# Kernel tuning notes

Measured on AMD Instinct MI355X. Metric: run time of the kernel, lower is better.

Reference implementation:

```python
import jax, jax.numpy as jnp
import numpy as np

ALPHA_POS, ALPHA_NEG, GAMMA, TAU = 1.0, 2.0, 2.0, 0.7
LAMBDA_CP, MU_ECE, N_BINS = 6.0, 5.0, 15
N = 16777216


def setup_inputs() -> dict:
    key = jax.random.key(0)
    k1, k2, k3 = jax.random.split(key, 3)
    p_hat = jax.random.uniform(k1, (N,), dtype=jnp.float32)
    u_hat = jax.random.uniform(k2, (N,), dtype=jnp.float32)
    targets = jax.random.randint(k3, (N,), 0, 2, dtype=jnp.int32)
    return {"p_hat": p_hat, "u_hat": u_hat, "targets": targets}


def _ece(probs, labels):
    # bin b covers (b/n_bins, (b+1)/n_bins]; single-pass histogram via segment_sum
    bins = jnp.clip(jnp.ceil(probs * N_BINS).astype(jnp.int32) - 1, 0, N_BINS - 1)
    sum_p = jax.ops.segment_sum(probs, bins, num_segments=N_BINS)
    sum_y = jax.ops.segment_sum(labels, bins, num_segments=N_BINS)
    # (|I_b|/N)*|mean_y - mean_p| == |sum_y - sum_p| / N ; empty bins contribute 0
    n = probs.shape[0]
    return jnp.sum(jnp.abs(sum_y - sum_p)) / n


def reference(p_hat, u_hat, targets):
    t = targets.astype(p_hat.dtype)
    pos = targets == 1
    pt = jnp.where(pos, p_hat, 1.0 - p_hat)
    alpha = jnp.where(pos, ALPHA_POS, ALPHA_NEG)
    focal = jnp.mean(-alpha * (1.0 - pt) ** GAMMA * jnp.log(pt + 1e-12))

    mask_ow = (~pos) & (p_hat > TAU)   # overconfident wrong
    mask_uc = pos & (p_hat < TAU)      # underconfident correct
    penalty = jnp.where(mask_ow, (1.0 - u_hat) ** 2,
                        jnp.where(mask_uc, u_hat ** 2, 0.0))
    cp_loss = jnp.mean(penalty)

    ece = _ece(p_hat, t)
    return focal + LAMBDA_CP * cp_loss + MU_ECE * ece
```

## Files before the change

### kernel.cpp

```cpp
#include <hip/hip_runtime.h>

#define NB 15
#define NV 17
#define GRID 1024
#define BLOCK 256


__device__ __forceinline__ void process_elem(float pk, float uk, int tk,
                                             float& facc, float& cacc,
                                             float* bins)
{
    bool pos = (tk == 1);

    float pt    = pos ? pk : 1.0f - pk;
    float alpha = pos ? 1.0f : 2.0f;
    float om    = 1.0f - pt;
    facc -= alpha * om * om * __logf(pt + 1e-12f);

    float w   = 1.0f - uk;
    float pen = pos ? ((pk < 0.7f) ? uk * uk : 0.0f)
                    : ((pk > 0.7f) ? w * w : 0.0f);
    cacc += pen;

    int b = (int)ceilf(pk * 15.0f) - 1;
    b = (b < 0) ? 0 : ((b > NB - 1) ? NB - 1 : b);
    float v = (pos ? 1.0f : 0.0f) - pk;
    #pragma unroll
    for (int j = 0; j < NB; ++j)
        bins[j] += (b == j) ? v : 0.0f;
}

__global__ __launch_bounds__(BLOCK) void fcl_main(
    const float* __restrict__ p_hat,
    const float* __restrict__ u_hat,
    const int*   __restrict__ targets,
    float* __restrict__ partials,
    int n4, int n)
{
    float bins[NB];
    #pragma unroll
    for (int j = 0; j < NB; ++j) bins[j] = 0.0f;
    float facc = 0.0f, cacc = 0.0f;

    const float4* __restrict__ p4 = (const float4*)p_hat;
    const float4* __restrict__ u4 = (const float4*)u_hat;
    const int4*   __restrict__ t4 = (const int4*)targets;

    const int stride = gridDim.x * blockDim.x;
    int i = blockIdx.x * blockDim.x + threadIdx.x;

    for (; i + stride < n4; i += 2 * stride) {
        float4 p0 = p4[i];          float4 p1 = p4[i + stride];
        float4 u0 = u4[i];          float4 u1 = u4[i + stride];
        int4   t0 = t4[i];          int4   t1 = t4[i + stride];
        #pragma unroll
        for (int k = 0; k < 4; ++k)
            process_elem((&p0.x)[k], (&u0.x)[k], (&t0.x)[k], facc, cacc, bins);
        #pragma unroll
        for (int k = 0; k < 4; ++k)
            process_elem((&p1.x)[k], (&u1.x)[k], (&t1.x)[k], facc, cacc, bins);
    }
    if (i < n4) {
        float4 p0 = p4[i]; float4 u0 = u4[i]; int4 t0 = t4[i];
        #pragma unroll
        for (int k = 0; k < 4; ++k)
            process_elem((&p0.x)[k], (&u0.x)[k], (&t0.x)[k], facc, cacc, bins);
    }

    if (blockIdx.x == 0 && threadIdx.x == 0) {
        for (int j = n4 * 4; j < n; ++j)
            process_elem(p_hat[j], u_hat[j], targets[j], facc, cacc, bins);
    }

    float vals[NV];
    vals[0] = facc; vals[1] = cacc;
    #pragma unroll
    for (int j = 0; j < NB; ++j) vals[2 + j] = bins[j];

    #pragma unroll
    for (int off = 32; off > 0; off >>= 1) {
        #pragma unroll
        for (int j = 0; j < NV; ++j)
            vals[j] += __shfl_down(vals[j], off, 64);
    }

    __shared__ float lds[BLOCK / 64][NV];
    const int wave = threadIdx.x >> 6;
    const int lane = threadIdx.x & 63;
    if (lane == 0) {
        #pragma unroll
        for (int j = 0; j < NV; ++j) lds[wave][j] = vals[j];
    }
    __syncthreads();

    if (threadIdx.x < NV) {
        float s = 0.0f;
        #pragma unroll
        for (int w = 0; w < BLOCK / 64; ++w) s += lds[w][threadIdx.x];
        partials[threadIdx.x * gridDim.x + blockIdx.x] = s;
    }
}

__global__ __launch_bounds__(1024) void fcl_final(
    const float* __restrict__ partials,
    float* __restrict__ out, float inv_n, int grid)
{
    const int t = threadIdx.x;
    float v[NV];
    #pragma unroll
    for (int j = 0; j < NV; ++j) v[j] = partials[j * grid + t];

    #pragma unroll
    for (int off = 32; off > 0; off >>= 1) {
        #pragma unroll
        for (int j = 0; j < NV; ++j)
            v[j] += __shfl_down(v[j], off, 64);
    }

    __shared__ float lds[16][NV];
    const int wave = t >> 6;
    const int lane = t & 63;
    if (lane == 0) {
        #pragma unroll
        for (int j = 0; j < NV; ++j) lds[wave][j] = v[j];
    }
    __syncthreads();

    if (t == 0) {
        float s[NV];
        #pragma unroll
        for (int j = 0; j < NV; ++j) s[j] = 0.0f;
        for (int w = 0; w < 16; ++w)
            #pragma unroll
            for (int j = 0; j < NV; ++j) s[j] += lds[w][j];
        float e = 0.0f;
        #pragma unroll
        for (int b = 0; b < NB; ++b) e += fabsf(s[2 + b]);
        out[0] = (s[0] + 6.0f * s[1] + 5.0f * e) * inv_n;
    }
}

extern "C" void kernel_launch(void* const* d_in, const int* in_sizes, int n_in,
                              void* d_out, int out_size, void* d_ws, size_t ws_size,
                              hipStream_t stream) {
    const float* p = (const float*)d_in[0];
    const float* u = (const float*)d_in[1];
    const int*   t = (const int*)d_in[2];
    float* out = (float*)d_out;
    float* ws  = (float*)d_ws;

    const int n  = in_sizes[0];
    const int n4 = n / 4;

    fcl_main<<<GRID, BLOCK, 0, stream>>>(p, u, t, ws, n4, n);
    fcl_final<<<1, 1024, 0, stream>>>(ws, out, 1.0f / (float)n, GRID);
}
```

Before: 205.0 us.

## Replace per-thread register bin accumulation with per-thread LDS atomics and enlarge grid

Per-element bin accumulation no longer does 15 predicated register adds. Each thread now keeps a private 15-float slice in shared memory and updates it with an LDS atomicAdd. The grid grows fourfold, so the final kernel now loops to sum more partials per thread. This trades ALU work for LDS traffic and atomic latency, and the 15 KB of shared memory per block may limit occupancy.

```diff
diff --git a/kernel.cpp b/kernel.cpp
--- a/kernel.cpp
+++ b/kernel.cpp
@@ -2,13 +2,13 @@
 
 #define NB 15
 #define NV 17
-#define GRID 1024
+#define GRID 4096
 #define BLOCK 256
 
 
 __device__ __forceinline__ void process_elem(float pk, float uk, int tk,
                                              float& facc, float& cacc,
-                                             float* bins)
+                                             float* __restrict__ lbins)
 {
     bool pos = (tk == 1);
 
@@ -25,9 +25,7 @@
     int b = (int)ceilf(pk * 15.0f) - 1;
     b = (b < 0) ? 0 : ((b > NB - 1) ? NB - 1 : b);
     float v = (pos ? 1.0f : 0.0f) - pk;
-    #pragma unroll
-    for (int j = 0; j < NB; ++j)
-        bins[j] += (b == j) ? v : 0.0f;
+    atomicAdd(&lbins[b], v);
 }
 
 __global__ __launch_bounds__(BLOCK) void fcl_main(
@@ -37,9 +35,11 @@
     float* __restrict__ partials,
     int n4, int n)
 {
-    float bins[NB];
-    #pragma unroll
-    for (int j = 0; j < NB; ++j) bins[j] = 0.0f;
+    __shared__ float sbins[BLOCK * NB];
+    for (int i = threadIdx.x; i < BLOCK * NB; i += BLOCK) sbins[i] = 0.0f;
+    __syncthreads();
+    float* __restrict__ lbins = &sbins[threadIdx.x * NB];
+
     float facc = 0.0f, cacc = 0.0f;
 
     const float4* __restrict__ p4 = (const float4*)p_hat;
@@ -55,27 +55,29 @@
         int4   t0 = t4[i];          int4   t1 = t4[i + stride];
         #pragma unroll
         for (int k = 0; k < 4; ++k)
-            process_elem((&p0.x)[k], (&u0.x)[k], (&t0.x)[k], facc, cacc, bins);
+            process_elem((&p0.x)[k], (&u0.x)[k], (&t0.x)[k], facc, cacc, lbins);
         #pragma unroll
         for (int k = 0; k < 4; ++k)
-            process_elem((&p1.x)[k], (&u1.x)[k], (&t1.x)[k], facc, cacc, bins);
+            process_elem((&p1.x)[k], (&u1.x)[k], (&t1.x)[k], facc, cacc, lbins);
     }
     if (i < n4) {
         float4 p0 = p4[i]; float4 u0 = u4[i]; int4 t0 = t4[i];
         #pragma unroll
         for (int k = 0; k < 4; ++k)
-            process_elem((&p0.x)[k], (&u0.x)[k], (&t0.x)[k], facc, cacc, bins);
+            process_elem((&p0.x)[k], (&u0.x)[k], (&t0.x)[k], facc, cacc, lbins);
     }
 
     if (blockIdx.x == 0 && threadIdx.x == 0) {
         for (int j = n4 * 4; j < n; ++j)
-            process_elem(p_hat[j], u_hat[j], targets[j], facc, cacc, bins);
+            process_elem(p_hat[j], u_hat[j], targets[j], facc, cacc, lbins);
     }
+
+    __syncthreads();
 
     float vals[NV];
     vals[0] = facc; vals[1] = cacc;
     #pragma unroll
-    for (int j = 0; j < NB; ++j) vals[2 + j] = bins[j];
+    for (int j = 0; j < NB; ++j) vals[2 + j] = lbins[j];
 
     #pragma unroll
     for (int off = 32; off > 0; off >>= 1) {
@@ -108,7 +110,11 @@
     const int t = threadIdx.x;
     float v[NV];
     #pragma unroll
-    for (int j = 0; j < NV; ++j) v[j] = partials[j * grid + t];
+    for (int j = 0; j < NV; ++j) {
+        float s = 0.0f;
+        for (int i = t; i < grid; i += 1024) s += partials[j * grid + i];
+        v[j] = s;
+    }
 
     #pragma unroll
     for (int off = 32; off > 0; off >>= 1) {
```

After: 258.4 us. 1.26x slower.
